# Kernel tuning notes

Measured on AMD Instinct MI355X. Metric: run time of the kernel, lower is better.

Reference implementation:

```python
import jax, jax.numpy as jnp
import numpy as np

B, S, D, H = 4, 2048, 1024, 16
DK = D // H

def setup_inputs() -> dict:
    key = jax.random.key(0)
    ks = jax.random.split(key, 8)
    query = jax.random.normal(ks[0], (B, S, D), dtype=jnp.float32)
    k_in = jax.random.normal(ks[1], (B, S, D), dtype=jnp.float32)
    v_in = jax.random.normal(ks[2], (B, S, D), dtype=jnp.float32)
    # causal mask: 1 where attending allowed, 0 masked (module masks where mask==0)
    mask = jnp.broadcast_to(jnp.tril(jnp.ones((S, S), dtype=jnp.int32)), (B, S, S))
    s = 1.0 / np.sqrt(D)
    w_q = jax.random.normal(ks[3], (D, D), dtype=jnp.float32) * s
    w_k = jax.random.normal(ks[4], (D, D), dtype=jnp.float32) * s
    w_v = jax.random.normal(ks[5], (D, D), dtype=jnp.float32) * s
    w_o = jax.random.normal(ks[6], (D, D), dtype=jnp.float32) * s
    b_o = jnp.zeros((D,), dtype=jnp.float32)
    return {"query": query, "key": k_in, "value": v_in, "mask": mask,
            "w_q": w_q, "w_k": w_k, "w_v": w_v, "w_o": w_o, "b_o": b_o}

def reference(query, key, value, mask, w_q, w_k, w_v, w_o, b_o):
    b, s, d = query.shape
    # projections (nn.Linear: x @ W.T); weights stored as [out, in]
    Q = (query @ w_q.T).reshape(b, s, H, DK).transpose(0, 2, 1, 3)  # [b,h,s,dk]
    K = (key   @ w_k.T).reshape(b, s, H, DK).transpose(0, 2, 1, 3)
    V = (value @ w_v.T).reshape(b, s, H, DK).transpose(0, 2, 1, 3)
    scores = jnp.einsum('bhqd,bhkd->bhqk', Q, K) / np.sqrt(DK)  # [b,h,s,s]
    m = mask[:, None, :, :]  # broadcast over heads
    scores = jnp.where(m == 0, jnp.float32(-1e9), scores)
    attn = jax.nn.softmax(scores, axis=-1)
    out = jnp.einsum('bhqk,bhkd->bhqd', attn, V)  # [b,h,s,dk]
    out = out.transpose(0, 2, 1, 3).reshape(b, s, d)
    out = out @ w_o.T + b_o
    return (out, attn)
```

## Files before the change

kernel.cpp:

```cpp
#include <hip/hip_runtime.h>
#include <hip/hip_bf16.h>

typedef __attribute__((ext_vector_type(8))) short bf16x8;
typedef __attribute__((ext_vector_type(4))) float f32x4;

constexpr int Bn = 4, Sn = 2048, Dn = 1024, Hn = 16;
constexpr int Mn = Bn * Sn;
constexpr float C_SCALE = 0.18033688f;

static __device__ __forceinline__ unsigned short f2bf(float f) {
  union { float f; unsigned int u; } v; v.f = f;
  unsigned int r = v.u + 0x7fffu + ((v.u >> 16) & 1u);
  return (unsigned short)(r >> 16);
}

static __device__ __forceinline__ void gload_lds16(const unsigned short* g,
                                                   unsigned short* l) {
  __builtin_amdgcn_global_load_lds(
      (const __attribute__((address_space(1))) unsigned int*)g,
      (__attribute__((address_space(3))) unsigned int*)l,
      16, 0, 0);
}

__global__ __launch_bounds__(256)
void cvt7(const float* __restrict__ q, const float* __restrict__ k,
          const float* __restrict__ v, const float* __restrict__ wq,
          const float* __restrict__ wk, const float* __restrict__ wv,
          const float* __restrict__ wo,
          unsigned short* __restrict__ oq, unsigned short* __restrict__ ok,
          unsigned short* __restrict__ ov, unsigned short* __restrict__ owq,
          unsigned short* __restrict__ owk, unsigned short* __restrict__ owv,
          unsigned short* __restrict__ owo)
{
  constexpr size_t NX = (size_t)Mn * Dn;
  constexpr size_t NW = (size_t)Dn * Dn;
  constexpr size_t total = 3 * NX + 4 * NW;
  size_t e = ((size_t)blockIdx.x * blockDim.x + threadIdx.x) * 4;
  const size_t step = (size_t)gridDim.x * blockDim.x * 4;
  for (; e < total; e += step) {
    int seg; size_t off;
    if (e < 3 * NX) { seg = (int)(e >> 23); off = e & (NX - 1); }
    else { const size_t j = e - 3 * NX; seg = 3 + (int)(j >> 20); off = j & (NW - 1); }
    const float* src; unsigned short* dst;
    switch (seg) {
      case 0: src = q;  dst = oq;  break;
      case 1: src = k;  dst = ok;  break;
      case 2: src = v;  dst = ov;  break;
      case 3: src = wq; dst = owq; break;
      case 4: src = wk; dst = owk; break;
      case 5: src = wv; dst = owv; break;
      default: src = wo; dst = owo; break;
    }
    const float4 val = *(const float4*)(src + off);
    ushort4 o;
    o.x = f2bf(val.x); o.y = f2bf(val.y); o.z = f2bf(val.z); o.w = f2bf(val.w);
    *(ushort4*)(dst + off) = o;
  }
}

static __device__ __forceinline__ void gemm_core(
    const unsigned short* __restrict__ A, const unsigned short* __restrict__ Bw,
    unsigned short* Asl, unsigned short* Bsl,
    int m0, int n0, int wave, int lane, f32x4 (*acc)[4])
{
  const int lr = lane & 15, lg = lane >> 4;
  const int wm = wave >> 1, wn = wave & 1;
  const int srow = wave * 32 + (lane >> 2);
  const int scol = (lane & 3) * 8;
  const unsigned short* ga0 = A  + (size_t)(m0 + srow) * 1024 + scol;
  const unsigned short* gb0 = Bw + (size_t)(n0 + srow) * 1024 + scol;

  for (int k0 = 0; k0 < 1024; k0 += 32) {
    __syncthreads();
    gload_lds16(ga0 + k0,             &Asl[(wave * 32) * 32]);
    gload_lds16(ga0 + k0 + 16 * 1024, &Asl[(wave * 32 + 16) * 32]);
    gload_lds16(gb0 + k0,             &Bsl[(wave * 32) * 32]);
    gload_lds16(gb0 + k0 + 16 * 1024, &Bsl[(wave * 32 + 16) * 32]);
    __syncthreads();

    bf16x8 af[4], bfr[4];
    #pragma unroll
    for (int mf = 0; mf < 4; ++mf)
      af[mf] = *(const bf16x8*)&Asl[(wm * 64 + mf * 16 + lr) * 32 + lg * 8];
    #pragma unroll
    for (int nf = 0; nf < 4; ++nf)
      bfr[nf] = *(const bf16x8*)&Bsl[(wn * 64 + nf * 16 + lr) * 32 + lg * 8];
    #pragma unroll
    for (int mf = 0; mf < 4; ++mf)
      #pragma unroll
      for (int nf = 0; nf < 4; ++nf)
        acc[mf][nf] = __builtin_amdgcn_mfma_f32_16x16x32_bf16(
            af[mf], bfr[nf], acc[mf][nf], 0, 0, 0);
  }
}

__global__ __launch_bounds__(256)
void gemm_qkv(const unsigned short* __restrict__ Xq,
              const unsigned short* __restrict__ Xk,
              const unsigned short* __restrict__ Xv,
              const unsigned short* __restrict__ Wq,
              const unsigned short* __restrict__ Wk,
              const unsigned short* __restrict__ Wv,
              unsigned short* __restrict__ Qbf,
              unsigned short* __restrict__ Kbf,
              unsigned short* __restrict__ Vtb)
{
  __shared__ unsigned short Asl[128 * 32];
  __shared__ unsigned short Bsl[128 * 32];
  __shared__ unsigned short Ts[128][136];

  const int tid  = threadIdx.x;
  const int wave = tid >> 6, lane = tid & 63;
  const int lr = lane & 15, lg = lane >> 4;
  const int wm = wave >> 1, wn = wave & 1;
  const int m0 = blockIdx.x * 128;
  const int n0 = blockIdx.y * 128;
  const int z  = blockIdx.z;

  const unsigned short* A  = (z == 0) ? Xq : (z == 1) ? Xk : Xv;
  const unsigned short* Bw = (z == 0) ? Wq : (z == 1) ? Wk : Wv;

  f32x4 acc[4][4] = {};
  gemm_core(A, Bw, Asl, Bsl, m0, n0, wave, lane, acc);

  if (z < 2) {
    unsigned short* C = (z == 0) ? Qbf : Kbf;
    const float cs = (z == 0) ? C_SCALE : 1.0f;
    #pragma unroll
    for (int mf = 0; mf < 4; ++mf)
      #pragma unroll
      for (int nf = 0; nf < 4; ++nf)
        #pragma unroll
        for (int i = 0; i < 4; ++i) {
          const int row = m0 + wm * 64 + mf * 16 + lg * 4 + i;
          const int col = n0 + wn * 64 + nf * 16 + lr;
          C[(size_t)row * 1024 + col] = f2bf(acc[mf][nf][i] * cs);
        }
  } else {
    #pragma unroll
    for (int mf = 0; mf < 4; ++mf)
      #pragma unroll
      for (int nf = 0; nf < 4; ++nf)
        #pragma unroll
        for (int i = 0; i < 4; ++i)
          Ts[wn * 64 + nf * 16 + lr][wm * 64 + mf * 16 + lg * 4 + i] =
              f2bf(acc[mf][nf][i]);
    __syncthreads();
    const int dkl = tid >> 1;
    const int sh  = (tid & 1) * 64;
    const int b = m0 >> 11, s0 = m0 & 2047;
    const int gcol = n0 + dkl;
    const int h = gcol >> 6, dk = gcol & 63;
    unsigned short* dst =
        Vtb + ((size_t)((b * 16 + h) * 64 + dk)) * Sn + s0 + sh;
    #pragma unroll
    for (int jj = 0; jj < 8; ++jj)
      *(bf16x8*)(dst + jj * 8) = *(const bf16x8*)&Ts[dkl][sh + jj * 8];
  }
}

__global__ __launch_bounds__(256)
void gemm_o(const unsigned short* __restrict__ A,
            const unsigned short* __restrict__ Bw,
            float* __restrict__ C, const float* __restrict__ bias)
{
  __shared__ unsigned short Asl[128 * 32];
  __shared__ unsigned short Bsl[128 * 32];
  const int tid  = threadIdx.x;
  const int wave = tid >> 6, lane = tid & 63;
  const int lr = lane & 15, lg = lane >> 4;
  const int wm = wave >> 1, wn = wave & 1;
  const int m0 = blockIdx.x * 128;
  const int n0 = blockIdx.y * 128;

  f32x4 acc[4][4] = {};
  gemm_core(A, Bw, Asl, Bsl, m0, n0, wave, lane, acc);

  float bv[4];
  #pragma unroll
  for (int nf = 0; nf < 4; ++nf) bv[nf] = bias[n0 + wn * 64 + nf * 16 + lr];
  #pragma unroll
  for (int mf = 0; mf < 4; ++mf)
    #pragma unroll
    for (int nf = 0; nf < 4; ++nf)
      #pragma unroll
      for (int i = 0; i < 4; ++i) {
        const int row = m0 + wm * 64 + mf * 16 + lg * 4 + i;
        const int col = n0 + wn * 64 + nf * 16 + lr;
        C[(size_t)row * 1024 + col] = acc[mf][nf][i] + bv[nf];
      }
}

__global__ __launch_bounds__(128)
void attn_fused(const unsigned short* __restrict__ Qb,
                const unsigned short* __restrict__ Kb,
                const unsigned short* __restrict__ Vt,
                float* __restrict__ attn_out,
                unsigned short* __restrict__ Ob)
{
  __shared__ unsigned short Ps[2][16][72];
  __shared__ float Pf[2][16][68];

  const int tid = threadIdx.x;
  const int w = tid >> 6, lane = tid & 63;
  const int lr = lane & 15, lg = lane >> 4;
  const int bh = blockIdx.x >> 6;
  const int j  = blockIdx.x & 63;
  const int qs = w ? (127 - j) : j;
  const int b = bh >> 4, h = bh & 15;
  const int q0 = qs * 16;
  const int nkt = (q0 + 15) / 64 + 1;
  const int kl  = nkt - 1;

  const unsigned short* Kbh = Kb + (size_t)(b * Sn) * Dn + h * 64;
  const unsigned short* Vbh = Vt + (size_t)(bh * 64) * Sn;
  float* aout = attn_out + (size_t)bh * Sn * (size_t)Sn;

  const int qoff = (b * Sn + q0 + lr) * Dn + h * 64 + lg * 8;
  bf16x8 qf[2];
  qf[0] = *(const bf16x8*)(Qb + qoff);
  qf[1] = *(const bf16x8*)(Qb + qoff + 32);

  float l[4] = {0.f, 0.f, 0.f, 0.f};

  for (int kt = 0; kt < kl; ++kt) {
    bf16x8 kf[4][2];
    #pragma unroll
    for (int nf = 0; nf < 4; ++nf)
      #pragma unroll
      for (int kk = 0; kk < 2; ++kk)
        kf[nf][kk] = *(const bf16x8*)(
            Kbh + (kt * 64 + nf * 16 + lr) * Dn + kk * 32 + lg * 8);
    f32x4 sf[4];
    #pragma unroll
    for (int nf = 0; nf < 4; ++nf) {
      f32x4 a = {0.f, 0.f, 0.f, 0.f};
      a = __builtin_amdgcn_mfma_f32_16x16x32_bf16(qf[0], kf[nf][0], a, 0, 0, 0);
      a = __builtin_amdgcn_mfma_f32_16x16x32_bf16(qf[1], kf[nf][1], a, 0, 0, 0);
      sf[nf] = a;
    }
    #pragma unroll
    for (int i = 0; i < 4; ++i)
      l[i] += (exp2f(sf[0][i]) + exp2f(sf[1][i])) +
              (exp2f(sf[2][i]) + exp2f(sf[3][i]));
  }
  {
    bf16x8 kf[4][2];
    #pragma unroll
    for (int nf = 0; nf < 4; ++nf)
      #pragma unroll
      for (int kk = 0; kk < 2; ++kk)
        kf[nf][kk] = *(const bf16x8*)(
            Kbh + (kl * 64 + nf * 16 + lr) * Dn + kk * 32 + lg * 8);
    f32x4 sf[4];
    #pragma unroll
    for (int nf = 0; nf < 4; ++nf) {
      f32x4 a = {0.f, 0.f, 0.f, 0.f};
      a = __builtin_amdgcn_mfma_f32_16x16x32_bf16(qf[0], kf[nf][0], a, 0, 0, 0);
      a = __builtin_amdgcn_mfma_f32_16x16x32_bf16(qf[1], kf[nf][1], a, 0, 0, 0);
      sf[nf] = a;
    }
    #pragma unroll
    for (int i = 0; i < 4; ++i) {
      const int q = q0 + lg * 4 + i;
      #pragma unroll
      for (int nf = 0; nf < 4; ++nf) {
        const int key = kl * 64 + nf * 16 + lr;
        l[i] += (key <= q) ? exp2f(sf[nf][i]) : 0.f;
      }
    }
  }
  #pragma unroll
  for (int i = 0; i < 4; ++i)
    #pragma unroll
    for (int d = 1; d < 16; d <<= 1) l[i] += __shfl_xor(l[i], d, 64);
  float nlg[4];
  #pragma unroll
  for (int i = 0; i < 4; ++i) nlg[i] = -log2f(l[i]);

  f32x4 oacc[4] = {};
  for (int kt = 0; kt < nkt; ++kt) {
    const bool last = (kt == kl);
    bf16x8 kf[4][2], vt[4][2];
    #pragma unroll
    for (int nf = 0; nf < 4; ++nf)
      #pragma unroll
      for (int kk = 0; kk < 2; ++kk) {
        kf[nf][kk] = *(const bf16x8*)(
            Kbh + (kt * 64 + nf * 16 + lr) * Dn + kk * 32 + lg * 8);
        vt[nf][kk] = *(const bf16x8*)(
            Vbh + (nf * 16 + lr) * Sn + kt * 64 + kk * 32 + lg * 8);
      }
    f32x4 sf[4];
    #pragma unroll
    for (int nf = 0; nf < 4; ++nf) {
      f32x4 a = {0.f, 0.f, 0.f, 0.f};
      a = __builtin_amdgcn_mfma_f32_16x16x32_bf16(qf[0], kf[nf][0], a, 0, 0, 0);
      a = __builtin_amdgcn_mfma_f32_16x16x32_bf16(qf[1], kf[nf][1], a, 0, 0, 0);
      sf[nf] = a;
    }
    if (!last) {
      #pragma unroll
      for (int nf = 0; nf < 4; ++nf)
        #pragma unroll
        for (int i = 0; i < 4; ++i) {
          const float p = exp2f(sf[nf][i] + nlg[i]);
          Pf[w][lg * 4 + i][nf * 16 + lr] = p;
          Ps[w][lg * 4 + i][nf * 16 + lr] = f2bf(p);
        }
    } else {
      #pragma unroll
      for (int nf = 0; nf < 4; ++nf)
        #pragma unroll
        for (int i = 0; i < 4; ++i) {
          const int q = q0 + lg * 4 + i;
          const int key = kl * 64 + nf * 16 + lr;
          float p = exp2f(sf[nf][i] + nlg[i]);
          if (key > q) p = 0.f;
          Pf[w][lg * 4 + i][nf * 16 + lr] = p;
          Ps[w][lg * 4 + i][nf * 16 + lr] = f2bf(p);
        }
    }
    #pragma unroll
    for (int jj = 0; jj < 4; ++jj) {
      const int r = jj * 4 + lg;
      const f32x4 pv = *(const f32x4*)&Pf[w][r][lr * 4];
      __builtin_nontemporal_store(
          pv, (f32x4*)&aout[(q0 + r) * Sn + kt * 64 + lr * 4]);
    }
    bf16x8 pa[2];
    pa[0] = *(const bf16x8*)&Ps[w][lr][lg * 8];
    pa[1] = *(const bf16x8*)&Ps[w][lr][32 + lg * 8];
    #pragma unroll
    for (int kk = 0; kk < 2; ++kk)
      #pragma unroll
      for (int nf = 0; nf < 4; ++nf)
        oacc[nf] = __builtin_amdgcn_mfma_f32_16x16x32_bf16(
            pa[kk], vt[nf][kk], oacc[nf], 0, 0, 0);
  }
  for (int kt = nkt; kt < Sn / 64; ++kt) {
    const f32x4 z = {0.f, 0.f, 0.f, 0.f};
    #pragma unroll
    for (int jj = 0; jj < 4; ++jj) {
      const int r = q0 + lg + 4 * jj;
      __builtin_nontemporal_store(
          z, (f32x4*)&aout[r * Sn + kt * 64 + lr * 4]);
    }
  }
  #pragma unroll
  for (int nf = 0; nf < 4; ++nf)
    #pragma unroll
    for (int i = 0; i < 4; ++i) {
      const int q = q0 + lg * 4 + i;
      const int dk = nf * 16 + lr;
      Ob[(b * Sn + q) * Dn + h * 64 + dk] = f2bf(oacc[nf][i]);
    }
}

extern "C" void kernel_launch(void* const* d_in, const int* in_sizes, int n_in,
                              void* d_out, int out_size, void* d_ws, size_t ws_size,
                              hipStream_t stream)
{
  const float* query = (const float*)d_in[0];
  const float* key   = (const float*)d_in[1];
  const float* value = (const float*)d_in[2];
  const float* w_q = (const float*)d_in[4];
  const float* w_k = (const float*)d_in[5];
  const float* w_v = (const float*)d_in[6];
  const float* w_o = (const float*)d_in[7];
  const float* b_o = (const float*)d_in[8];

  constexpr size_t NX = (size_t)Mn * Dn;
  constexpr size_t NW = (size_t)Dn * Dn;
  unsigned short* Xq  = (unsigned short*)d_ws;
  unsigned short* Xk  = Xq  + NX;
  unsigned short* Xv  = Xk  + NX;
  unsigned short* Wq  = Xv  + NX;
  unsigned short* Wk  = Wq  + NW;
  unsigned short* Wv  = Wk  + NW;
  unsigned short* Wo  = Wv  + NW;
  unsigned short* Qbf = Wo  + NW;
  unsigned short* Kbf = Qbf + NX;
  unsigned short* Vtb = Kbf + NX;
  unsigned short* Obf = Vtb + NX;

  float* out  = (float*)d_out;
  float* attn = out + NX;

  cvt7<<<dim3(2048), dim3(256), 0, stream>>>(query, key, value, w_q, w_k, w_v, w_o,
                                             Xq, Xk, Xv, Wq, Wk, Wv, Wo);
  gemm_qkv<<<dim3(Mn / 128, Dn / 128, 3), dim3(256), 0, stream>>>(
      Xq, Xk, Xv, Wq, Wk, Wv, Qbf, Kbf, Vtb);
  attn_fused<<<dim3(64 * 64), dim3(128), 0, stream>>>(Qbf, Kbf, Vtb, attn, Obf);
  gemm_o<<<dim3(Mn / 128, Dn / 128), dim3(256), 0, stream>>>(Obf, Wo, out, b_o);
}
```

Before: 554.1 us.

## Move causal attn zero-fill into QKV GEMM launch as extra block role

Zero-filling the masked upper triangle of the attention matrix moves out of the attention kernel and into extra blocks of the QKV projection launch. The grid is flattened so every fourth block zeros attn rows instead of doing GEMM work, letting the large store-bound fill overlap with compute-bound GEMM blocks. LDS buffers are merged into one shared buffer, with an added barrier before the V transpose reuses it. The risk is that zero-fill blocks compete for bandwidth and change the GEMM block scheduling order.

```diff
diff --git a/kernel.cpp b/kernel.cpp
--- a/kernel.cpp
+++ b/kernel.cpp
@@ -103,19 +103,43 @@
               const unsigned short* __restrict__ Wv,
               unsigned short* __restrict__ Qbf,
               unsigned short* __restrict__ Kbf,
-              unsigned short* __restrict__ Vtb)
-{
-  __shared__ unsigned short Asl[128 * 32];
-  __shared__ unsigned short Bsl[128 * 32];
-  __shared__ unsigned short Ts[128][136];
+              unsigned short* __restrict__ Vtb,
+              float* __restrict__ attn_out)
+{
+  __shared__ unsigned short ShBuf[128 * 136];
+  unsigned short* Asl = ShBuf;
+  unsigned short* Bsl = ShBuf + 128 * 32;
 
   const int tid  = threadIdx.x;
+  const int role = blockIdx.x & 3;
+  const int tile = blockIdx.x >> 2;
+
+  if (role == 3) {
+    const int bh = tile >> 3;
+    const int c  = tile & 7;
+    float* aout = attn_out + (size_t)bh * Sn * (size_t)Sn;
+    const f32x4 zz = {0.f, 0.f, 0.f, 0.f};
+    #pragma unroll
+    for (int a = 0; a < 4; ++a) {
+      const int qt = c + 8 * a;
+      const int col0 = 64 * (qt + 1);
+      const int nv = (Sn - col0) >> 2;
+      if (nv <= 0) continue;
+      for (int r = 0; r < 64; ++r) {
+        float* rowp = aout + (size_t)(qt * 64 + r) * Sn + col0;
+        for (int t = tid; t < nv; t += 256)
+          __builtin_nontemporal_store(zz, (f32x4*)(rowp + t * 4));
+      }
+    }
+    return;
+  }
+
   const int wave = tid >> 6, lane = tid & 63;
   const int lr = lane & 15, lg = lane >> 4;
   const int wm = wave >> 1, wn = wave & 1;
-  const int m0 = blockIdx.x * 128;
-  const int n0 = blockIdx.y * 128;
-  const int z  = blockIdx.z;
+  const int m0 = (tile >> 3) * 128;
+  const int n0 = (tile & 7) * 128;
+  const int z  = role;
 
   const unsigned short* A  = (z == 0) ? Xq : (z == 1) ? Xk : Xv;
   const unsigned short* Bw = (z == 0) ? Wq : (z == 1) ? Wk : Wv;
@@ -137,6 +161,8 @@
           C[(size_t)row * 1024 + col] = f2bf(acc[mf][nf][i] * cs);
         }
   } else {
+    unsigned short (*Ts)[136] = (unsigned short (*)[136])ShBuf;
+    __syncthreads();
     #pragma unroll
     for (int mf = 0; mf < 4; ++mf)
       #pragma unroll
@@ -337,15 +363,6 @@
       for (int nf = 0; nf < 4; ++nf)
         oacc[nf] = __builtin_amdgcn_mfma_f32_16x16x32_bf16(
             pa[kk], vt[nf][kk], oacc[nf], 0, 0, 0);
-  }
-  for (int kt = nkt; kt < Sn / 64; ++kt) {
-    const f32x4 z = {0.f, 0.f, 0.f, 0.f};
-    #pragma unroll
-    for (int jj = 0; jj < 4; ++jj) {
-      const int r = q0 + lg + 4 * jj;
-      __builtin_nontemporal_store(
-          z, (f32x4*)&aout[r * Sn + kt * 64 + lr * 4]);
-    }
   }
   #pragma unroll
   for (int nf = 0; nf < 4; ++nf)
@@ -389,8 +406,8 @@
 
   cvt7<<<dim3(2048), dim3(256), 0, stream>>>(query, key, value, w_q, w_k, w_v, w_o,
                                              Xq, Xk, Xv, Wq, Wk, Wv, Wo);
-  gemm_qkv<<<dim3(Mn / 128, Dn / 128, 3), dim3(256), 0, stream>>>(
-      Xq, Xk, Xv, Wq, Wk, Wv, Qbf, Kbf, Vtb);
+  gemm_qkv<<<dim3(2048), dim3(256), 0, stream>>>(
+      Xq, Xk, Xv, Wq, Wk, Wv, Qbf, Kbf, Vtb, attn);
   attn_fused<<<dim3(64 * 64), dim3(128), 0, stream>>>(Qbf, Kbf, Vtb, attn, Obf);
   gemm_o<<<dim3(Mn / 128, Dn / 128), dim3(256), 0, stream>>>(Obf, Wo, out, b_o);
 }
```

Result: slower. 688.2 us (+24.2%).

## Compute transposed QK^T so each lane owns one query row, drop fp32 LDS staging

Applied to the files above, without the earlier changes.

Swaps the MFMA operands so the score tile comes out transposed: each lane holds four consecutive keys for a single query. The row-sum then needs only two cross-lane shuffles instead of sixteen, and probabilities can be written straight to global memory as float4 without staging through an fp32 LDS buffer. The bf16 copy for the PV MFMA is packed with the hardware v_cvt_pk_bf16_f32 instruction and written to LDS as 8-byte chunks with a new padding. This cuts LDS traffic and VALU work, but the global stores now come from a different per-lane layout, and the packed conversion may round differently from the old software routine.

```diff
diff --git a/kernel.cpp b/kernel.cpp
--- a/kernel.cpp
+++ b/kernel.cpp
@@ -12,6 +12,12 @@
   union { float f; unsigned int u; } v; v.f = f;
   unsigned int r = v.u + 0x7fffu + ((v.u >> 16) & 1u);
   return (unsigned short)(r >> 16);
+}
+
+static __device__ __forceinline__ unsigned int cvtpk_bf16(float lo, float hi) {
+  unsigned int r;
+  asm("v_cvt_pk_bf16_f32 %0, %1, %2" : "=v"(r) : "v"(lo), "v"(hi));
+  return r;
 }
 
 static __device__ __forceinline__ void gload_lds16(const unsigned short* g,
@@ -198,8 +204,7 @@
                 float* __restrict__ attn_out,
                 unsigned short* __restrict__ Ob)
 {
-  __shared__ unsigned short Ps[2][16][72];
-  __shared__ float Pf[2][16][68];
+  __shared__ unsigned short Ps[2][16][88];
 
   const int tid = threadIdx.x;
   const int w = tid >> 6, lane = tid & 63;
@@ -216,12 +221,13 @@
   const unsigned short* Vbh = Vt + (size_t)(bh * 64) * Sn;
   float* aout = attn_out + (size_t)bh * Sn * (size_t)Sn;
 
-  const int qoff = (b * Sn + q0 + lr) * Dn + h * 64 + lg * 8;
+  const int q = q0 + lr;
+  const int qoff = (b * Sn + q) * Dn + h * 64 + lg * 8;
   bf16x8 qf[2];
   qf[0] = *(const bf16x8*)(Qb + qoff);
   qf[1] = *(const bf16x8*)(Qb + qoff + 32);
 
-  float l[4] = {0.f, 0.f, 0.f, 0.f};
+  float l = 0.f;
 
   for (int kt = 0; kt < kl; ++kt) {
     bf16x8 kf[4][2];
@@ -231,18 +237,13 @@
       for (int kk = 0; kk < 2; ++kk)
         kf[nf][kk] = *(const bf16x8*)(
             Kbh + (kt * 64 + nf * 16 + lr) * Dn + kk * 32 + lg * 8);
-    f32x4 sf[4];
     #pragma unroll
     for (int nf = 0; nf < 4; ++nf) {
       f32x4 a = {0.f, 0.f, 0.f, 0.f};
-      a = __builtin_amdgcn_mfma_f32_16x16x32_bf16(qf[0], kf[nf][0], a, 0, 0, 0);
-      a = __builtin_amdgcn_mfma_f32_16x16x32_bf16(qf[1], kf[nf][1], a, 0, 0, 0);
-      sf[nf] = a;
-    }
-    #pragma unroll
-    for (int i = 0; i < 4; ++i)
-      l[i] += (exp2f(sf[0][i]) + exp2f(sf[1][i])) +
-              (exp2f(sf[2][i]) + exp2f(sf[3][i]));
+      a = __builtin_amdgcn_mfma_f32_16x16x32_bf16(kf[nf][0], qf[0], a, 0, 0, 0);
+      a = __builtin_amdgcn_mfma_f32_16x16x32_bf16(kf[nf][1], qf[1], a, 0, 0, 0);
+      l += (exp2f(a[0]) + exp2f(a[1])) + (exp2f(a[2]) + exp2f(a[3]));
+    }
   }
   {
     bf16x8 kf[4][2];
@@ -252,31 +253,21 @@
       for (int kk = 0; kk < 2; ++kk)
         kf[nf][kk] = *(const bf16x8*)(
             Kbh + (kl * 64 + nf * 16 + lr) * Dn + kk * 32 + lg * 8);
-    f32x4 sf[4];
     #pragma unroll
     for (int nf = 0; nf < 4; ++nf) {
       f32x4 a = {0.f, 0.f, 0.f, 0.f};
-      a = __builtin_amdgcn_mfma_f32_16x16x32_bf16(qf[0], kf[nf][0], a, 0, 0, 0);
-      a = __builtin_amdgcn_mfma_f32_16x16x32_bf16(qf[1], kf[nf][1], a, 0, 0, 0);
-      sf[nf] = a;
-    }
-    #pragma unroll
-    for (int i = 0; i < 4; ++i) {
-      const int q = q0 + lg * 4 + i;
-      #pragma unroll
-      for (int nf = 0; nf < 4; ++nf) {
-        const int key = kl * 64 + nf * 16 + lr;
-        l[i] += (key <= q) ? exp2f(sf[nf][i]) : 0.f;
+      a = __builtin_amdgcn_mfma_f32_16x16x32_bf16(kf[nf][0], qf[0], a, 0, 0, 0);
+      a = __builtin_amdgcn_mfma_f32_16x16x32_bf16(kf[nf][1], qf[1], a, 0, 0, 0);
+      #pragma unroll
+      for (int i = 0; i < 4; ++i) {
+        const int key = kl * 64 + nf * 16 + lg * 4 + i;
+        l += (key <= q) ? exp2f(a[i]) : 0.f;
       }
     }
   }
-  #pragma unroll
-  for (int i = 0; i < 4; ++i)
-    #pragma unroll
-    for (int d = 1; d < 16; d <<= 1) l[i] += __shfl_xor(l[i], d, 64);
-  float nlg[4];
-  #pragma unroll
-  for (int i = 0; i < 4; ++i) nlg[i] = -log2f(l[i]);
+  l += __shfl_xor(l, 16, 64);
+  l += __shfl_xor(l, 32, 64);
+  const float nlg = -log2f(l);
 
   f32x4 oacc[4] = {};
   for (int kt = 0; kt < nkt; ++kt) {
@@ -291,42 +282,29 @@
         vt[nf][kk] = *(const bf16x8*)(
             Vbh + (nf * 16 + lr) * Sn + kt * 64 + kk * 32 + lg * 8);
       }
-    f32x4 sf[4];
     #pragma unroll
     for (int nf = 0; nf < 4; ++nf) {
       f32x4 a = {0.f, 0.f, 0.f, 0.f};
-      a = __builtin_amdgcn_mfma_f32_16x16x32_bf16(qf[0], kf[nf][0], a, 0, 0, 0);
-      a = __builtin_amdgcn_mfma_f32_16x16x32_bf16(qf[1], kf[nf][1], a, 0, 0, 0);
-      sf[nf] = a;
-    }
-    if (!last) {
-      #pragma unroll
-      for (int nf = 0; nf < 4; ++nf)
+      a = __builtin_amdgcn_mfma_f32_16x16x32_bf16(kf[nf][0], qf[0], a, 0, 0, 0);
+      a = __builtin_amdgcn_mfma_f32_16x16x32_bf16(kf[nf][1], qf[1], a, 0, 0, 0);
+      f32x4 p4;
+      if (!last) {
+        #pragma unroll
+        for (int i = 0; i < 4; ++i) p4[i] = exp2f(a[i] + nlg);
+      } else {
         #pragma unroll
         for (int i = 0; i < 4; ++i) {
-          const float p = exp2f(sf[nf][i] + nlg[i]);
-          Pf[w][lg * 4 + i][nf * 16 + lr] = p;
-          Ps[w][lg * 4 + i][nf * 16 + lr] = f2bf(p);
+          const int key = kl * 64 + nf * 16 + lg * 4 + i;
+          const float v = exp2f(a[i] + nlg);
+          p4[i] = (key <= q) ? v : 0.f;
         }
-    } else {
-      #pragma unroll
-      for (int nf = 0; nf < 4; ++nf)
-        #pragma unroll
-        for (int i = 0; i < 4; ++i) {
-          const int q = q0 + lg * 4 + i;
-          const int key = kl * 64 + nf * 16 + lr;
-          float p = exp2f(sf[nf][i] + nlg[i]);
-          if (key > q) p = 0.f;
-          Pf[w][lg * 4 + i][nf * 16 + lr] = p;
-          Ps[w][lg * 4 + i][nf * 16 + lr] = f2bf(p);
-        }
-    }
-    #pragma unroll
-    for (int jj = 0; jj < 4; ++jj) {
-      const int r = jj * 4 + lg;
-      const f32x4 pv = *(const f32x4*)&Pf[w][r][lr * 4];
+      }
       __builtin_nontemporal_store(
-          pv, (f32x4*)&aout[(q0 + r) * Sn + kt * 64 + lr * 4]);
+          p4, (f32x4*)&aout[q * Sn + kt * 64 + nf * 16 + lg * 4]);
+      uint2 pk;
+      pk.x = cvtpk_bf16(p4[0], p4[1]);
+      pk.y = cvtpk_bf16(p4[2], p4[3]);
+      *(uint2*)&Ps[w][lr][nf * 16 + lg * 4] = pk;
     }
     bf16x8 pa[2];
     pa[0] = *(const bf16x8*)&Ps[w][lr][lg * 8];
@@ -351,9 +329,9 @@
   for (int nf = 0; nf < 4; ++nf)
     #pragma unroll
     for (int i = 0; i < 4; ++i) {
-      const int q = q0 + lg * 4 + i;
+      const int qq = q0 + lg * 4 + i;
       const int dk = nf * 16 + lr;
-      Ob[(b * Sn + q) * Dn + h * 64 + dk] = f2bf(oacc[nf][i]);
+      Ob[(b * Sn + qq) * Dn + h * 64 + dk] = f2bf(oacc[nf][i]);
     }
 }
 
```

After: 564.4 us. About the same (+1.9%).
